# Performance work log

Hardware: AMD Instinct MI355X
Metric: run time of the kernel (lower is better)

Reference implementation:

```python
import jax, jax.numpy as jnp
import numpy as np

B, L, N, P = 64, 512, 321, 720   # batch, seq_len, enc_in, pred_len
E, R, CID, H = 8, 32, 32, 64     # experts, rank, channel_identity_dim, router hidden


def setup_inputs() -> dict:
    key = jax.random.key(0)
    ks = jax.random.split(key, 9)
    return {
        "x": jax.random.normal(ks[0], (B, L, N), dtype=jnp.float32),
        # per-channel identity embedding for the router
        "ident": jax.random.normal(ks[1], (N, CID), dtype=jnp.float32) * 0.02,
        # router MLP: CID -> H -> E
        "rw1": jax.random.normal(ks[2], (CID, H), dtype=jnp.float32) * (1.0 / np.sqrt(CID)),
        "rb1": jnp.zeros((H,), dtype=jnp.float32),
        "rw2": jax.random.normal(ks[3], (H, E), dtype=jnp.float32) * (1.0 / np.sqrt(H)),
        "rb2": jnp.zeros((E,), dtype=jnp.float32),
        # low-rank experts: L -> R -> P
        "w1": jax.random.normal(ks[4], (E, L, R), dtype=jnp.float32) * (1.0 / np.sqrt(L)),
        "w2": jax.random.normal(ks[5], (E, R, P), dtype=jnp.float32) * (1.0 / np.sqrt(R)),
        "b": jnp.zeros((E, P), dtype=jnp.float32),
    }


def reference(x, ident, rw1, rb1, rw2, rb2, w1, w2, b):
    # RevIN-style normalization over the time dim (torch std is unbiased, ddof=1)
    mean = jnp.mean(x, axis=1, keepdims=True)                    # [B,1,N]
    std = jnp.std(x, axis=1, keepdims=True, ddof=1) + 1e-6       # [B,1,N]
    xn = ((x - mean) / std).transpose(0, 2, 1)                   # [B,N,L]

    # per-channel MoE router (soft routing over experts)
    hidden = jax.nn.relu(ident @ rw1 + rb1)                      # [N,H]
    gate = jax.nn.softmax(hidden @ rw2 + rb2, axis=-1)           # [N,E]

    # low-rank expert projections L -> R -> P
    h = jnp.einsum('bnl,elr->bner', xn, w1)                      # [B,N,E,R]
    y = jnp.einsum('bner,erp->bnep', h, w2) + b                  # [B,N,E,P]
    y = jnp.einsum('bnep,ne->bnp', y, gate)                      # [B,N,P]

    pred = y.transpose(0, 2, 1)                                  # [B,P,N]
    return pred * std + mean
```

## Files before the change

kernel.cpp:

```cpp
#include <hip/hip_runtime.h>
#include <math.h>

#define B_ 64
#define L_ 512
#define N_ 321
#define P_ 720
#define E_ 8
#define R_ 32
#define CID_ 32
#define H_ 64
#define ER_ 256
#define KB2 288
#define HGROWS 384

typedef __attribute__((ext_vector_type(8))) short bf16x8;
typedef __attribute__((ext_vector_type(4))) float f32x4;
typedef __attribute__((ext_vector_type(8))) unsigned short u16x8;
typedef __attribute__((ext_vector_type(4))) unsigned short u16x4;

#define OFF_GATE 0
#define OFF_CS1  2568
#define OFF_W1K  2824
#define OFF_W2X  68360
#define OFF_HG   172040

__device__ __forceinline__ unsigned short f2bf(float f) {
    unsigned u = __float_as_uint(f);
    u += 0x7fffu + ((u >> 16) & 1u);
    return (unsigned short)(u >> 16);
}
__device__ __forceinline__ float bf2f(unsigned short h) {
    return __uint_as_float(((unsigned)h) << 16);
}

__global__ void router_kernel(const float* __restrict__ ident,
                              const float* __restrict__ rw1, const float* __restrict__ rb1,
                              const float* __restrict__ rw2, const float* __restrict__ rb2,
                              float* __restrict__ gate) {
    int n = blockIdx.x;
    int t = threadIdx.x;
    __shared__ float hid[H_];
    __shared__ float lg[E_];
    float acc = rb1[t];
    #pragma unroll
    for (int c = 0; c < CID_; ++c)
        acc = fmaf(ident[n*CID_ + c], rw1[c*H_ + t], acc);
    hid[t] = fmaxf(acc, 0.f);
    __syncthreads();
    if (t < E_) {
        float a = rb2[t];
        #pragma unroll
        for (int h = 0; h < H_; ++h) a = fmaf(hid[h], rw2[h*E_ + t], a);
        lg[t] = a;
    }
    __syncthreads();
    if (t == 0) {
        float m = lg[0];
        #pragma unroll
        for (int e = 1; e < E_; ++e) m = fmaxf(m, lg[e]);
        float s = 0.f, ex[E_];
        #pragma unroll
        for (int e = 0; e < E_; ++e) { ex[e] = expf(lg[e] - m); s += ex[e]; }
        float inv = 1.f / s;
        #pragma unroll
        for (int e = 0; e < E_; ++e) gate[n*E_ + e] = ex[e] * inv;
    }
}

__global__ void prep_kernel(const float* __restrict__ w1, const float* __restrict__ w2,
                            const float* __restrict__ bias,
                            unsigned short* __restrict__ w1k, unsigned short* __restrict__ w2x,
                            float* __restrict__ cs1) {
    __shared__ float red[16][32];
    int bid = blockIdx.x, t = threadIdx.x;
    if (bid < 128) {
        #pragma unroll
        for (int r = 0; r < 2; ++r) {
            int g = bid*1024 + r*512 + t;
            int er = g >> 9, l = g & 511;
            w1k[g] = f2bf(w1[(size_t)(er >> 5)*(L_*R_) + (size_t)l*R_ + (er & 31)]);
        }
    } else if (bid < 848) {
        int p = bid - 128;
        if (t < KB2) {
            unsigned short v;
            if (t < ER_)            v = f2bf(w2[(size_t)t*P_ + p]);
            else if (t < ER_ + E_)  v = f2bf(bias[(size_t)(t - ER_)*P_ + p]);
            else if (t == ER_ + E_) v = 0x3f80;
            else                    v = 0;
            w2x[(size_t)p*KB2 + t] = v;
        }
    } else {
        int e = bid - 848;
        int q = t >> 5, r = t & 31;
        float s = 0.f;
        for (int l = q; l < L_; l += 16)
            s += bf2f(f2bf(w1[(size_t)e*(L_*R_) + (size_t)l*R_ + r]));
        red[q][r] = s;
        __syncthreads();
        if (q == 0) {
            #pragma unroll
            for (int qq = 1; qq < 16; ++qq) s += red[qq][r];
            cs1[e*32 + r] = s;
        }
    }
}

__global__ __launch_bounds__(512, 4) void gemm1_kernel(
        const float* __restrict__ x, const unsigned short* __restrict__ w1k,
        const float* __restrict__ gate, const float* __restrict__ cs1,
        unsigned short* __restrict__ hg) {
    __shared__ unsigned short buf[2][64][128];
    __shared__ float red1[8][64], red2[8][64];
    __shared__ float meanS[64], sdS[64];

    const int bid = blockIdx.x;
    const int xcd = bid & 7;
    const int idx = bid >> 3;
    const int b   = (xcd << 3) + idx / 6;
    const int n0  = (idx % 6) * 64;

    const int tid  = threadIdx.x;
    const int lane = tid & 63;
    const int wave = tid >> 6;
    const int l15  = lane & 15;
    const int kgrp = lane >> 4;

    const int xn  = lane;
    const int gn  = n0 + xn;
    const int gnc = (gn < N_) ? gn : (N_ - 1);
    const float* xp = x + (size_t)b*L_*N_ + gnc;
    const int swz = (xn & 7) << 4;
    char* myrow0 = (char*)&buf[0][xn][0];
    char* myrow1 = (char*)&buf[1][xn][0];

    const unsigned short* apA = w1k + (size_t)(wave*32 + l15)*L_;
    const unsigned short* apB = w1k + (size_t)(wave*32 + 16 + l15)*L_;
    const int rsw = (l15 & 7) << 4;

    float s1 = 0.f, s2 = 0.f;
    float v[16];
    f32x4 acc[2][4];
    #pragma unroll
    for (int i = 0; i < 2; ++i)
        #pragma unroll
        for (int j = 0; j < 4; ++j) acc[i][j] = (f32x4){0.f,0.f,0.f,0.f};

#define LOADV(rd_) {                                                            \
    const int kb = (rd_)*128 + wave*16;                                         \
    _Pragma("unroll")                                                           \
    for (int i_ = 0; i_ < 16; ++i_)                                             \
        v[i_] = xp[(size_t)(kb + i_)*N_]; }
#define STOREV(rd_) {                                                           \
    char* dst = ((rd_) & 1) ? myrow1 : myrow0;                                  \
    u16x8 pk0, pk1;                                                             \
    _Pragma("unroll")                                                           \
    for (int i_ = 0; i_ < 8; ++i_) {                                            \
        s1 += v[i_]; s2 = fmaf(v[i_], v[i_], s2); pk0[i_] = f2bf(v[i_]); }      \
    _Pragma("unroll")                                                           \
    for (int i_ = 0; i_ < 8; ++i_) {                                            \
        float f_ = v[8+i_];                                                     \
        s1 += f_; s2 = fmaf(f_, f_, s2); pk1[i_] = f2bf(f_); }                  \
    *(u16x8*)(dst + ((wave*32)      ^ swz)) = pk0;                              \
    *(u16x8*)(dst + ((wave*32 + 16) ^ swz)) = pk1; }

    LOADV(0);
    STOREV(0);
    __syncthreads();

    bf16x8 af[4][2];
#define LDA(s_, kk_) { af[s_][0] = *(const bf16x8*)&apA[(kk_)*32 + kgrp*8];      \
                       af[s_][1] = *(const bf16x8*)&apB[(kk_)*32 + kgrp*8]; }
    LDA(0, 0); LDA(1, 1);

    #pragma unroll
    for (int rd = 0; rd < 4; ++rd) {
        if (rd < 3) LOADV(rd + 1);
        const unsigned short (*cb)[128] = buf[rd & 1];
        #pragma unroll
        for (int ks = 0; ks < 4; ++ks) {
            const int kk = rd*4 + ks;
            if (kk + 2 < 16) LDA((kk + 2) & 3, kk + 2);
            const int cbyte = ks*64 + kgrp*16;
            bf16x8 bfr[4];
            #pragma unroll
            for (int fn = 0; fn < 4; ++fn)
                bfr[fn] = *(const bf16x8*)((const char*)&cb[fn*16 + l15][0] + (cbyte ^ rsw));
            #pragma unroll
            for (int fn = 0; fn < 4; ++fn) {
                acc[0][fn] = __builtin_amdgcn_mfma_f32_16x16x32_bf16(af[kk & 3][0], bfr[fn], acc[0][fn], 0, 0, 0);
                acc[1][fn] = __builtin_amdgcn_mfma_f32_16x16x32_bf16(af[kk & 3][1], bfr[fn], acc[1][fn], 0, 0, 0);
            }
        }
        if (rd < 3) STOREV(rd + 1);
        __syncthreads();
    }
#undef LDA
#undef LOADV
#undef STOREV

    red1[wave][xn] = s1;
    red2[wave][xn] = s2;
    __syncthreads();
    if (tid < 64) {
        float a = 0.f, qq = 0.f;
        #pragma unroll
        for (int kk = 0; kk < 8; ++kk) { a += red1[kk][tid]; qq += red2[kk][tid]; }
        float mean = a * (1.f/L_);
        float var = (qq - (float)L_*mean*mean) * (1.f/(L_-1));
        var = fmaxf(var, 0.f);
        meanS[tid] = mean;
        sdS[tid]   = sqrtf(var) + 1e-6f;
    }
    __syncthreads();

    unsigned short* hgb = hg + ((size_t)b * HGROWS + n0) * KB2;
    #pragma unroll
    for (int fm = 0; fm < 2; ++fm) {
        int er0 = wave*32 + fm*16 + kgrp*4;
        int e = er0 >> 5;
        f32x4 c4 = *(const f32x4*)&cs1[er0];
        #pragma unroll
        for (int fn = 0; fn < 4; ++fn) {
            int nl = fn*16 + l15;
            int gnn = n0 + nl; if (gnn > N_-1) gnn = N_-1;
            float g = gate[gnn*E_ + e];
            float m = meanS[nl];
            u16x4 pk;
            #pragma unroll
            for (int j = 0; j < 4; ++j)
                pk[j] = f2bf(g * (acc[fm][fn][j] - m * c4[j]));
            *(u16x4*)&hgb[(size_t)nl*KB2 + er0] = pk;
        }
    }
    {
        int nl = tid >> 3, seg = tid & 7;
        int gnn = n0 + nl; if (gnn > N_-1) gnn = N_-1;
        float sd = sdS[nl], m = meanS[nl];
        u16x4 pk;
        #pragma unroll
        for (int jj = 0; jj < 4; ++jj) {
            int k = seg*4 + jj;
            float vv = (k < E_) ? gate[gnn*E_ + k] * sd : ((k == E_) ? m : 0.f);
            pk[jj] = f2bf(vv);
        }
        *(u16x4*)&hgb[(size_t)nl*KB2 + ER_ + seg*4] = pk;
    }
}

#define HGS 296
__global__ __launch_bounds__(512, 6) void gemm2_kernel(
        const unsigned short* __restrict__ hg, const unsigned short* __restrict__ w2x,
        float* __restrict__ out) {
    __shared__ __align__(16) char smem[64 * HGS * 2];
    unsigned short* hgL = (unsigned short*)smem;
    const int bid = blockIdx.x;
    const int xcd = bid & 7;
    const int idx = bid >> 3;
    const int b   = (xcd << 3) + idx / 36;
    const int rem = idx % 36;
    const int p0  = (rem / 6) * 128;
    const int n0  = (rem % 6) * 64;

    const int tid  = threadIdx.x;
    const int lane = tid & 63;
    const int wave = tid >> 6;
    const int l15  = lane & 15;
    const int kgrp = lane >> 4;

    const unsigned short* hgb = hg + ((size_t)b * HGROWS + n0) * KB2;
    #pragma unroll
    for (int it = 0; it < 5; ++it) {
        int c = tid + it*512;
        if (c < 64*36) {
            int row = c / 36, col = c % 36;
            *(u16x8*)&hgL[(size_t)row*HGS + col*8] =
                *(const u16x8*)&hgb[(size_t)row*KB2 + col*8];
        }
    }
    __syncthreads();

    int prow = p0 + wave*16 + l15; if (prow > P_-1) prow = P_-1;
    const unsigned short* ap = w2x + (size_t)prow*KB2;
    f32x4 o[4];
    #pragma unroll
    for (int j = 0; j < 4; ++j) o[j] = (f32x4){0.f,0.f,0.f,0.f};
    #pragma unroll
    for (int ks = 0; ks < 9; ++ks) {
        bf16x8 afr = *(const bf16x8*)&ap[ks*32 + kgrp*8];
        #pragma unroll
        for (int fn = 0; fn < 4; ++fn) {
            bf16x8 bfr = *(const bf16x8*)&hgL[(size_t)(fn*16 + l15)*HGS + ks*32 + kgrp*8];
            o[fn] = __builtin_amdgcn_mfma_f32_16x16x32_bf16(afr, bfr, o[fn], 0, 0, 0);
        }
    }
    __syncthreads();

    float* patch = (float*)smem + wave * 1088;
    #pragma unroll
    for (int fn = 0; fn < 4; ++fn)
        #pragma unroll
        for (int j = 0; j < 4; ++j)
            patch[(kgrp*4 + j)*68 + fn*16 + l15] = o[fn][j];
    const int pw0 = p0 + wave*16;
    #pragma unroll
    for (int pass = 0; pass < 4; ++pass) {
        int ploc = pass*4 + kgrp;
        f32x4 v = *(const f32x4*)&patch[ploc*68 + l15*4];
        int p = pw0 + ploc;
        int n = n0 + l15*4;
        if (p < P_) {
            float* orow = out + ((size_t)b*P_ + p)*N_;
            if (n + 3 < N_) {
                *(f32x4*)&orow[n] = v;
            } else {
                #pragma unroll
                for (int j = 0; j < 4; ++j)
                    if (n + j < N_) orow[n + j] = v[j];
            }
        }
    }
}

extern "C" void kernel_launch(void* const* d_in, const int* in_sizes, int n_in,
                              void* d_out, int out_size, void* d_ws, size_t ws_size,
                              hipStream_t stream) {
    const float* x     = (const float*)d_in[0];
    const float* ident = (const float*)d_in[1];
    const float* rw1   = (const float*)d_in[2];
    const float* rb1   = (const float*)d_in[3];
    const float* rw2   = (const float*)d_in[4];
    const float* rb2   = (const float*)d_in[5];
    const float* w1    = (const float*)d_in[6];
    const float* w2    = (const float*)d_in[7];
    const float* bias  = (const float*)d_in[8];
    float* out = (float*)d_out;
    float* ws  = (float*)d_ws;

    float* gate = ws + OFF_GATE;
    float* cs1  = ws + OFF_CS1;
    unsigned short* w1k = (unsigned short*)(ws + OFF_W1K);
    unsigned short* w2x = (unsigned short*)(ws + OFF_W2X);
    unsigned short* hg  = (unsigned short*)(ws + OFF_HG);

    router_kernel<<<N_, 64, 0, stream>>>(ident, rw1, rb1, rw2, rb2, gate);
    prep_kernel<<<856, 512, 0, stream>>>(w1, w2, bias, w1k, w2x, cs1);
    gemm1_kernel<<<dim3(384), 512, 0, stream>>>(x, w1k, gate, cs1, hg);
    gemm2_kernel<<<dim3(2304), 512, 0, stream>>>(hg, w2x, out);
}
```

Before: 66.61 us.

## Fuse router into prep kernel and split gemm1 across expert halves

The router computation moves into extra blocks of the prep kernel, which removes one kernel launch. gemm1 now splits the 256 expert-rank outputs into two halves of 128 across separate blocks, giving 768 blocks instead of 384. The accumulators per thread are halved and launch bounds allow 6 blocks per CU, which is meant to raise occupancy and parallelism. The cost is that each block now reloads and re-reduces the x tile, so reads of x and the mean/std work are duplicated.

```diff
diff --git a/kernel.cpp b/kernel.cpp
--- a/kernel.cpp
+++ b/kernel.cpp
@@ -33,45 +33,16 @@
     return __uint_as_float(((unsigned)h) << 16);
 }
 
-__global__ void router_kernel(const float* __restrict__ ident,
-                              const float* __restrict__ rw1, const float* __restrict__ rb1,
-                              const float* __restrict__ rw2, const float* __restrict__ rb2,
-                              float* __restrict__ gate) {
-    int n = blockIdx.x;
-    int t = threadIdx.x;
+__global__ void prep_kernel(const float* __restrict__ w1, const float* __restrict__ w2,
+                            const float* __restrict__ bias,
+                            const float* __restrict__ ident,
+                            const float* __restrict__ rw1, const float* __restrict__ rb1,
+                            const float* __restrict__ rw2, const float* __restrict__ rb2,
+                            unsigned short* __restrict__ w1k, unsigned short* __restrict__ w2x,
+                            float* __restrict__ cs1, float* __restrict__ gate) {
+    __shared__ float red[16][32];
     __shared__ float hid[H_];
     __shared__ float lg[E_];
-    float acc = rb1[t];
-    #pragma unroll
-    for (int c = 0; c < CID_; ++c)
-        acc = fmaf(ident[n*CID_ + c], rw1[c*H_ + t], acc);
-    hid[t] = fmaxf(acc, 0.f);
-    __syncthreads();
-    if (t < E_) {
-        float a = rb2[t];
-        #pragma unroll
-        for (int h = 0; h < H_; ++h) a = fmaf(hid[h], rw2[h*E_ + t], a);
-        lg[t] = a;
-    }
-    __syncthreads();
-    if (t == 0) {
-        float m = lg[0];
-        #pragma unroll
-        for (int e = 1; e < E_; ++e) m = fmaxf(m, lg[e]);
-        float s = 0.f, ex[E_];
-        #pragma unroll
-        for (int e = 0; e < E_; ++e) { ex[e] = expf(lg[e] - m); s += ex[e]; }
-        float inv = 1.f / s;
-        #pragma unroll
-        for (int e = 0; e < E_; ++e) gate[n*E_ + e] = ex[e] * inv;
-    }
-}
-
-__global__ void prep_kernel(const float* __restrict__ w1, const float* __restrict__ w2,
-                            const float* __restrict__ bias,
-                            unsigned short* __restrict__ w1k, unsigned short* __restrict__ w2x,
-                            float* __restrict__ cs1) {
-    __shared__ float red[16][32];
     int bid = blockIdx.x, t = threadIdx.x;
     if (bid < 128) {
         #pragma unroll
@@ -90,7 +61,7 @@
             else                    v = 0;
             w2x[(size_t)p*KB2 + t] = v;
         }
-    } else {
+    } else if (bid < 856) {
         int e = bid - 848;
         int q = t >> 5, r = t & 31;
         float s = 0.f;
@@ -103,10 +74,38 @@
             for (int qq = 1; qq < 16; ++qq) s += red[qq][r];
             cs1[e*32 + r] = s;
         }
-    }
-}
-
-__global__ __launch_bounds__(512, 4) void gemm1_kernel(
+    } else {
+        int n = bid - 856;
+        if (t < H_) {
+            float acc = rb1[t];
+            #pragma unroll
+            for (int c = 0; c < CID_; ++c)
+                acc = fmaf(ident[n*CID_ + c], rw1[c*H_ + t], acc);
+            hid[t] = fmaxf(acc, 0.f);
+        }
+        __syncthreads();
+        if (t < E_) {
+            float a = rb2[t];
+            #pragma unroll
+            for (int h = 0; h < H_; ++h) a = fmaf(hid[h], rw2[h*E_ + t], a);
+            lg[t] = a;
+        }
+        __syncthreads();
+        if (t == 0) {
+            float m = lg[0];
+            #pragma unroll
+            for (int e = 1; e < E_; ++e) m = fmaxf(m, lg[e]);
+            float s = 0.f, ex[E_];
+            #pragma unroll
+            for (int e = 0; e < E_; ++e) { ex[e] = expf(lg[e] - m); s += ex[e]; }
+            float inv = 1.f / s;
+            #pragma unroll
+            for (int e = 0; e < E_; ++e) gate[n*E_ + e] = ex[e] * inv;
+        }
+    }
+}
+
+__global__ __launch_bounds__(512, 6) void gemm1_kernel(
         const float* __restrict__ x, const unsigned short* __restrict__ w1k,
         const float* __restrict__ gate, const float* __restrict__ cs1,
         unsigned short* __restrict__ hg) {
@@ -117,8 +116,12 @@
     const int bid = blockIdx.x;
     const int xcd = bid & 7;
     const int idx = bid >> 3;
-    const int b   = (xcd << 3) + idx / 6;
-    const int n0  = (idx % 6) * 64;
+    const int b   = (xcd << 3) + idx / 12;
+    const int rem = idx % 12;
+    const int nt  = rem >> 1;
+    const int eq  = rem & 1;
+    const int n0  = nt * 64;
+    const int m0  = eq * 128;
 
     const int tid  = threadIdx.x;
     const int lane = tid & 63;
@@ -134,17 +137,14 @@
     char* myrow0 = (char*)&buf[0][xn][0];
     char* myrow1 = (char*)&buf[1][xn][0];
 
-    const unsigned short* apA = w1k + (size_t)(wave*32 + l15)*L_;
-    const unsigned short* apB = w1k + (size_t)(wave*32 + 16 + l15)*L_;
+    const unsigned short* apA = w1k + (size_t)(m0 + wave*16 + l15)*L_;
     const int rsw = (l15 & 7) << 4;
 
     float s1 = 0.f, s2 = 0.f;
     float v[16];
-    f32x4 acc[2][4];
-    #pragma unroll
-    for (int i = 0; i < 2; ++i)
-        #pragma unroll
-        for (int j = 0; j < 4; ++j) acc[i][j] = (f32x4){0.f,0.f,0.f,0.f};
+    f32x4 acc[4];
+    #pragma unroll
+    for (int j = 0; j < 4; ++j) acc[j] = (f32x4){0.f,0.f,0.f,0.f};
 
 #define LOADV(rd_) {                                                            \
     const int kb = (rd_)*128 + wave*16;                                         \
@@ -168,9 +168,8 @@
     STOREV(0);
     __syncthreads();
 
-    bf16x8 af[4][2];
-#define LDA(s_, kk_) { af[s_][0] = *(const bf16x8*)&apA[(kk_)*32 + kgrp*8];      \
-                       af[s_][1] = *(const bf16x8*)&apB[(kk_)*32 + kgrp*8]; }
+    bf16x8 af[4];
+#define LDA(s_, kk_) af[s_] = *(const bf16x8*)&apA[(kk_)*32 + kgrp*8];
     LDA(0, 0); LDA(1, 1);
 
     #pragma unroll
@@ -187,10 +186,8 @@
             for (int fn = 0; fn < 4; ++fn)
                 bfr[fn] = *(const bf16x8*)((const char*)&cb[fn*16 + l15][0] + (cbyte ^ rsw));
             #pragma unroll
-            for (int fn = 0; fn < 4; ++fn) {
-                acc[0][fn] = __builtin_amdgcn_mfma_f32_16x16x32_bf16(af[kk & 3][0], bfr[fn], acc[0][fn], 0, 0, 0);
-                acc[1][fn] = __builtin_amdgcn_mfma_f32_16x16x32_bf16(af[kk & 3][1], bfr[fn], acc[1][fn], 0, 0, 0);
-            }
+            for (int fn = 0; fn < 4; ++fn)
+                acc[fn] = __builtin_amdgcn_mfma_f32_16x16x32_bf16(af[kk & 3], bfr[fn], acc[fn], 0, 0, 0);
         }
         if (rd < 3) STOREV(rd + 1);
         __syncthreads();
@@ -215,9 +212,8 @@
     __syncthreads();
 
     unsigned short* hgb = hg + ((size_t)b * HGROWS + n0) * KB2;
-    #pragma unroll
-    for (int fm = 0; fm < 2; ++fm) {
-        int er0 = wave*32 + fm*16 + kgrp*4;
+    {
+        int er0 = m0 + wave*16 + kgrp*4;
         int e = er0 >> 5;
         f32x4 c4 = *(const f32x4*)&cs1[er0];
         #pragma unroll
@@ -229,11 +225,11 @@
             u16x4 pk;
             #pragma unroll
             for (int j = 0; j < 4; ++j)
-                pk[j] = f2bf(g * (acc[fm][fn][j] - m * c4[j]));
+                pk[j] = f2bf(g * (acc[fn][j] - m * c4[j]));
             *(u16x4*)&hgb[(size_t)nl*KB2 + er0] = pk;
         }
     }
-    {
+    if (eq == 1) {
         int nl = tid >> 3, seg = tid & 7;
         int gnn = n0 + nl; if (gnn > N_-1) gnn = N_-1;
         float sd = sdS[nl], m = meanS[nl];
@@ -343,8 +339,8 @@
     unsigned short* w2x = (unsigned short*)(ws + OFF_W2X);
     unsigned short* hg  = (unsigned short*)(ws + OFF_HG);
 
-    router_kernel<<<N_, 64, 0, stream>>>(ident, rw1, rb1, rw2, rb2, gate);
-    prep_kernel<<<856, 512, 0, stream>>>(w1, w2, bias, w1k, w2x, cs1);
-    gemm1_kernel<<<dim3(384), 512, 0, stream>>>(x, w1k, gate, cs1, hg);
+    prep_kernel<<<856 + N_, 512, 0, stream>>>(w1, w2, bias, ident, rw1, rb1,
+                                              rw2, rb2, w1k, w2x, cs1, gate);
+    gemm1_kernel<<<dim3(768), 512, 0, stream>>>(x, w1k, gate, cs1, hg);
     gemm2_kernel<<<dim3(2304), 512, 0, stream>>>(hg, w2x, out);
 }
```

New measurement: 60.97 us. 8.5% less time.

## Pre-transpose x to bf16 in a separate kernel and merge router into prep

Applied to the files above, without the earlier changes.

Adds a kernel that transposes x from [B,L,N] into a bf16 [B,384,L] buffer through padded shared memory, so gemm1 can read contiguous rows instead of strided columns. gemm1 then loads each 32-channel tile in one pass, computes the mean/std with shuffles and runs a single unpipelined MFMA loop over 704 blocks. The router kernel is folded into the prep kernel as extra blocks, removing one launch. The change adds an extra bf16 copy of x written to and read back from global memory. Statistics are now computed from bf16-rounded values rather than fp32.

```diff
diff --git a/kernel.cpp b/kernel.cpp
--- a/kernel.cpp
+++ b/kernel.cpp
@@ -12,17 +12,20 @@
 #define ER_ 256
 #define KB2 288
 #define HGROWS 384
+#define TRS 338
 
 typedef __attribute__((ext_vector_type(8))) short bf16x8;
 typedef __attribute__((ext_vector_type(4))) float f32x4;
 typedef __attribute__((ext_vector_type(8))) unsigned short u16x8;
 typedef __attribute__((ext_vector_type(4))) unsigned short u16x4;
+typedef __attribute__((ext_vector_type(2))) unsigned short u16x2;
 
 #define OFF_GATE 0
 #define OFF_CS1  2568
 #define OFF_W1K  2824
 #define OFF_W2X  68360
-#define OFF_HG   172040
+#define OFF_XT   172040
+#define OFF_HG   6463496
 
 __device__ __forceinline__ unsigned short f2bf(float f) {
     unsigned u = __float_as_uint(f);
@@ -33,45 +36,16 @@
     return __uint_as_float(((unsigned)h) << 16);
 }
 
-__global__ void router_kernel(const float* __restrict__ ident,
-                              const float* __restrict__ rw1, const float* __restrict__ rb1,
-                              const float* __restrict__ rw2, const float* __restrict__ rb2,
-                              float* __restrict__ gate) {
-    int n = blockIdx.x;
-    int t = threadIdx.x;
+__global__ void prep_kernel(const float* __restrict__ w1, const float* __restrict__ w2,
+                            const float* __restrict__ bias,
+                            const float* __restrict__ ident,
+                            const float* __restrict__ rw1, const float* __restrict__ rb1,
+                            const float* __restrict__ rw2, const float* __restrict__ rb2,
+                            unsigned short* __restrict__ w1k, unsigned short* __restrict__ w2x,
+                            float* __restrict__ cs1, float* __restrict__ gate) {
+    __shared__ float red[16][32];
     __shared__ float hid[H_];
     __shared__ float lg[E_];
-    float acc = rb1[t];
-    #pragma unroll
-    for (int c = 0; c < CID_; ++c)
-        acc = fmaf(ident[n*CID_ + c], rw1[c*H_ + t], acc);
-    hid[t] = fmaxf(acc, 0.f);
-    __syncthreads();
-    if (t < E_) {
-        float a = rb2[t];
-        #pragma unroll
-        for (int h = 0; h < H_; ++h) a = fmaf(hid[h], rw2[h*E_ + t], a);
-        lg[t] = a;
-    }
-    __syncthreads();
-    if (t == 0) {
-        float m = lg[0];
-        #pragma unroll
-        for (int e = 1; e < E_; ++e) m = fmaxf(m, lg[e]);
-        float s = 0.f, ex[E_];
-        #pragma unroll
-        for (int e = 0; e < E_; ++e) { ex[e] = expf(lg[e] - m); s += ex[e]; }
-        float inv = 1.f / s;
-        #pragma unroll
-        for (int e = 0; e < E_; ++e) gate[n*E_ + e] = ex[e] * inv;
-    }
-}
-
-__global__ void prep_kernel(const float* __restrict__ w1, const float* __restrict__ w2,
-                            const float* __restrict__ bias,
-                            unsigned short* __restrict__ w1k, unsigned short* __restrict__ w2x,
-                            float* __restrict__ cs1) {
-    __shared__ float red[16][32];
     int bid = blockIdx.x, t = threadIdx.x;
     if (bid < 128) {
         #pragma unroll
@@ -90,7 +64,7 @@
             else                    v = 0;
             w2x[(size_t)p*KB2 + t] = v;
         }
-    } else {
+    } else if (bid < 856) {
         int e = bid - 848;
         int q = t >> 5, r = t & 31;
         float s = 0.f;
@@ -103,22 +77,92 @@
             for (int qq = 1; qq < 16; ++qq) s += red[qq][r];
             cs1[e*32 + r] = s;
         }
+    } else {
+        int n = bid - 856;
+        if (t < H_) {
+            float acc = rb1[t];
+            #pragma unroll
+            for (int c = 0; c < CID_; ++c)
+                acc = fmaf(ident[n*CID_ + c], rw1[c*H_ + t], acc);
+            hid[t] = fmaxf(acc, 0.f);
+        }
+        __syncthreads();
+        if (t < E_) {
+            float a = rb2[t];
+            #pragma unroll
+            for (int h = 0; h < H_; ++h) a = fmaf(hid[h], rw2[h*E_ + t], a);
+            lg[t] = a;
+        }
+        __syncthreads();
+        if (t == 0) {
+            float m = lg[0];
+            #pragma unroll
+            for (int e = 1; e < E_; ++e) m = fmaxf(m, lg[e]);
+            float s = 0.f, ex[E_];
+            #pragma unroll
+            for (int e = 0; e < E_; ++e) { ex[e] = expf(lg[e] - m); s += ex[e]; }
+            float inv = 1.f / s;
+            #pragma unroll
+            for (int e = 0; e < E_; ++e) gate[n*E_ + e] = ex[e] * inv;
+        }
+    }
+}
+
+__global__ __launch_bounds__(512) void prepx2_kernel(
+        const float* __restrict__ x, unsigned short* __restrict__ xT) {
+    __shared__ unsigned short tr[64 * TRS];
+    const int bid = blockIdx.x;
+    const int b   = bid >> 3;
+    const int kc  = bid & 7;
+    const int tid = threadIdx.x;
+    const int lane = tid & 63;
+    const int wave = tid >> 6;
+
+    const float* xb = x + (size_t)b*L_*N_ + (size_t)kc*64*N_;
+    #pragma unroll
+    for (int rr = 0; rr < 8; ++rr) {
+        const int r = wave*8 + rr;
+        const float* row = xb + (size_t)r*N_;
+        #pragma unroll
+        for (int it = 0; it < 6; ++it) {
+            int c = it*64 + lane;
+            if (c < N_)        tr[r*TRS + c] = f2bf(row[c]);
+            else if (c < 336)  tr[r*TRS + c] = 0;
+        }
+    }
+    __syncthreads();
+
+    #pragma unroll
+    for (int pass = 0; pass < 6; ++pass) {
+        int n = pass*64 + (tid >> 3);
+        int chunk = tid & 7;
+        if (n < 336) {
+            u16x8 pk;
+            #pragma unroll
+            for (int j = 0; j < 8; ++j) pk[j] = tr[(chunk*8 + j)*TRS + n];
+            *(u16x8*)&xT[((size_t)b*HGROWS + n)*L_ + kc*64 + chunk*8] = pk;
+        }
+    }
+    if (tid < 384) {
+        int n = 336 + (tid >> 3);
+        int chunk = tid & 7;
+        u16x8 z = {0,0,0,0,0,0,0,0};
+        *(u16x8*)&xT[((size_t)b*HGROWS + n)*L_ + kc*64 + chunk*8] = z;
     }
 }
 
 __global__ __launch_bounds__(512, 4) void gemm1_kernel(
-        const float* __restrict__ x, const unsigned short* __restrict__ w1k,
+        const unsigned short* __restrict__ xT, const unsigned short* __restrict__ w1k,
         const float* __restrict__ gate, const float* __restrict__ cs1,
         unsigned short* __restrict__ hg) {
-    __shared__ unsigned short buf[2][64][128];
-    __shared__ float red1[8][64], red2[8][64];
-    __shared__ float meanS[64], sdS[64];
+    __shared__ __align__(16) unsigned short xL[32 * 512];
+    __shared__ float meanS[32], sdS[32];
 
     const int bid = blockIdx.x;
     const int xcd = bid & 7;
     const int idx = bid >> 3;
-    const int b   = (xcd << 3) + idx / 6;
-    const int n0  = (idx % 6) * 64;
+    const int b   = (xcd << 3) + idx / 11;
+    const int n0  = (idx % 11) * 32;
 
     const int tid  = threadIdx.x;
     const int lane = tid & 63;
@@ -126,93 +170,67 @@
     const int l15  = lane & 15;
     const int kgrp = lane >> 4;
 
-    const int xn  = lane;
-    const int gn  = n0 + xn;
-    const int gnc = (gn < N_) ? gn : (N_ - 1);
-    const float* xp = x + (size_t)b*L_*N_ + gnc;
-    const int swz = (xn & 7) << 4;
-    char* myrow0 = (char*)&buf[0][xn][0];
-    char* myrow1 = (char*)&buf[1][xn][0];
+    const int n_loc = tid >> 4;
+    const int seg   = tid & 15;
+    const unsigned short* xrow = xT + ((size_t)b*HGROWS + n0 + n_loc)*L_ + seg*32;
+    float s1 = 0.f, s2 = 0.f;
+    {
+        u16x8 st[4];
+        #pragma unroll
+        for (int j = 0; j < 4; ++j) {
+            st[j] = *(const u16x8*)&xrow[j*8];
+            #pragma unroll
+            for (int q = 0; q < 8; ++q) {
+                float f = bf2f(st[j][q]);
+                s1 += f; s2 = fmaf(f, f, s2);
+            }
+        }
+        const int swzw = (n_loc & 7) << 4;
+        char* dst = (char*)xL + n_loc*1024;
+        #pragma unroll
+        for (int j = 0; j < 4; ++j)
+            *(u16x8*)(dst + ((seg*64 + j*16) ^ swzw)) = st[j];
+    }
+    __syncthreads();
+    #pragma unroll
+    for (int m = 1; m <= 8; m <<= 1) {
+        s1 += __shfl_xor(s1, m);
+        s2 += __shfl_xor(s2, m);
+    }
+    if (seg == 0) {
+        float mean = s1 * (1.f/L_);
+        float var = (s2 - (float)L_*mean*mean) * (1.f/(L_-1));
+        meanS[n_loc] = mean;
+        sdS[n_loc]   = sqrtf(fmaxf(var, 0.f)) + 1e-6f;
+    }
+    __syncthreads();
 
     const unsigned short* apA = w1k + (size_t)(wave*32 + l15)*L_;
     const unsigned short* apB = w1k + (size_t)(wave*32 + 16 + l15)*L_;
     const int rsw = (l15 & 7) << 4;
 
-    float s1 = 0.f, s2 = 0.f;
-    float v[16];
-    f32x4 acc[2][4];
+    f32x4 acc[2][2];
     #pragma unroll
     for (int i = 0; i < 2; ++i)
         #pragma unroll
-        for (int j = 0; j < 4; ++j) acc[i][j] = (f32x4){0.f,0.f,0.f,0.f};
-
-#define LOADV(rd_) {                                                            \
-    const int kb = (rd_)*128 + wave*16;                                         \
-    _Pragma("unroll")                                                           \
-    for (int i_ = 0; i_ < 16; ++i_)                                             \
-        v[i_] = xp[(size_t)(kb + i_)*N_]; }
-#define STOREV(rd_) {                                                           \
-    char* dst = ((rd_) & 1) ? myrow1 : myrow0;                                  \
-    u16x8 pk0, pk1;                                                             \
-    _Pragma("unroll")                                                           \
-    for (int i_ = 0; i_ < 8; ++i_) {                                            \
-        s1 += v[i_]; s2 = fmaf(v[i_], v[i_], s2); pk0[i_] = f2bf(v[i_]); }      \
-    _Pragma("unroll")                                                           \
-    for (int i_ = 0; i_ < 8; ++i_) {                                            \
-        float f_ = v[8+i_];                                                     \
-        s1 += f_; s2 = fmaf(f_, f_, s2); pk1[i_] = f2bf(f_); }                  \
-    *(u16x8*)(dst + ((wave*32)      ^ swz)) = pk0;                              \
-    *(u16x8*)(dst + ((wave*32 + 16) ^ swz)) = pk1; }
-
-    LOADV(0);
-    STOREV(0);
-    __syncthreads();
+        for (int j = 0; j < 2; ++j) acc[i][j] = (f32x4){0.f,0.f,0.f,0.f};
 
     bf16x8 af[4][2];
 #define LDA(s_, kk_) { af[s_][0] = *(const bf16x8*)&apA[(kk_)*32 + kgrp*8];      \
                        af[s_][1] = *(const bf16x8*)&apB[(kk_)*32 + kgrp*8]; }
     LDA(0, 0); LDA(1, 1);
-
-    #pragma unroll
-    for (int rd = 0; rd < 4; ++rd) {
-        if (rd < 3) LOADV(rd + 1);
-        const unsigned short (*cb)[128] = buf[rd & 1];
-        #pragma unroll
-        for (int ks = 0; ks < 4; ++ks) {
-            const int kk = rd*4 + ks;
-            if (kk + 2 < 16) LDA((kk + 2) & 3, kk + 2);
-            const int cbyte = ks*64 + kgrp*16;
-            bf16x8 bfr[4];
-            #pragma unroll
-            for (int fn = 0; fn < 4; ++fn)
-                bfr[fn] = *(const bf16x8*)((const char*)&cb[fn*16 + l15][0] + (cbyte ^ rsw));
-            #pragma unroll
-            for (int fn = 0; fn < 4; ++fn) {
-                acc[0][fn] = __builtin_amdgcn_mfma_f32_16x16x32_bf16(af[kk & 3][0], bfr[fn], acc[0][fn], 0, 0, 0);
-                acc[1][fn] = __builtin_amdgcn_mfma_f32_16x16x32_bf16(af[kk & 3][1], bfr[fn], acc[1][fn], 0, 0, 0);
-            }
-        }
-        if (rd < 3) STOREV(rd + 1);
-        __syncthreads();
+    #pragma unroll
+    for (int ks = 0; ks < 16; ++ks) {
+        if (ks + 2 < 16) LDA((ks + 2) & 3, ks + 2);
+        const int cb = (ks*64 + kgrp*16);
+        bf16x8 b0 = *(const bf16x8*)((char*)xL + l15*1024        + (cb ^ rsw));
+        bf16x8 b1 = *(const bf16x8*)((char*)xL + (16 + l15)*1024 + (cb ^ rsw));
+        acc[0][0] = __builtin_amdgcn_mfma_f32_16x16x32_bf16(af[ks & 3][0], b0, acc[0][0], 0, 0, 0);
+        acc[0][1] = __builtin_amdgcn_mfma_f32_16x16x32_bf16(af[ks & 3][0], b1, acc[0][1], 0, 0, 0);
+        acc[1][0] = __builtin_amdgcn_mfma_f32_16x16x32_bf16(af[ks & 3][1], b0, acc[1][0], 0, 0, 0);
+        acc[1][1] = __builtin_amdgcn_mfma_f32_16x16x32_bf16(af[ks & 3][1], b1, acc[1][1], 0, 0, 0);
     }
 #undef LDA
-#undef LOADV
-#undef STOREV
-
-    red1[wave][xn] = s1;
-    red2[wave][xn] = s2;
-    __syncthreads();
-    if (tid < 64) {
-        float a = 0.f, qq = 0.f;
-        #pragma unroll
-        for (int kk = 0; kk < 8; ++kk) { a += red1[kk][tid]; qq += red2[kk][tid]; }
-        float mean = a * (1.f/L_);
-        float var = (qq - (float)L_*mean*mean) * (1.f/(L_-1));
-        var = fmaxf(var, 0.f);
-        meanS[tid] = mean;
-        sdS[tid]   = sqrtf(var) + 1e-6f;
-    }
-    __syncthreads();
 
     unsigned short* hgb = hg + ((size_t)b * HGROWS + n0) * KB2;
     #pragma unroll
@@ -221,7 +239,7 @@
         int e = er0 >> 5;
         f32x4 c4 = *(const f32x4*)&cs1[er0];
         #pragma unroll
-        for (int fn = 0; fn < 4; ++fn) {
+        for (int fn = 0; fn < 2; ++fn) {
             int nl = fn*16 + l15;
             int gnn = n0 + nl; if (gnn > N_-1) gnn = N_-1;
             float g = gate[gnn*E_ + e];
@@ -234,17 +252,17 @@
         }
     }
     {
-        int nl = tid >> 3, seg = tid & 7;
+        int nl = tid >> 4, sg = tid & 15;
         int gnn = n0 + nl; if (gnn > N_-1) gnn = N_-1;
         float sd = sdS[nl], m = meanS[nl];
-        u16x4 pk;
-        #pragma unroll
-        for (int jj = 0; jj < 4; ++jj) {
-            int k = seg*4 + jj;
+        u16x2 pk;
+        #pragma unroll
+        for (int jj = 0; jj < 2; ++jj) {
+            int k = sg*2 + jj;
             float vv = (k < E_) ? gate[gnn*E_ + k] * sd : ((k == E_) ? m : 0.f);
             pk[jj] = f2bf(vv);
         }
-        *(u16x4*)&hgb[(size_t)nl*KB2 + ER_ + seg*4] = pk;
+        *(u16x2*)&hgb[(size_t)nl*KB2 + ER_ + sg*2] = pk;
     }
 }
 
@@ -341,10 +359,12 @@
     float* cs1  = ws + OFF_CS1;
     unsigned short* w1k = (unsigned short*)(ws + OFF_W1K);
     unsigned short* w2x = (unsigned short*)(ws + OFF_W2X);
+    unsigned short* xT  = (unsigned short*)(ws + OFF_XT);
     unsigned short* hg  = (unsigned short*)(ws + OFF_HG);
 
-    router_kernel<<<N_, 64, 0, stream>>>(ident, rw1, rb1, rw2, rb2, gate);
-    prep_kernel<<<856, 512, 0, stream>>>(w1, w2, bias, w1k, w2x, cs1);
-    gemm1_kernel<<<dim3(384), 512, 0, stream>>>(x, w1k, gate, cs1, hg);
+    prep_kernel<<<856 + N_, 512, 0, stream>>>(w1, w2, bias, ident, rw1, rb1,
+                                              rw2, rb2, w1k, w2x, cs1, gate);
+    prepx2_kernel<<<512, 512, 0, stream>>>(x, xT);
+    gemm1_kernel<<<dim3(704), 512, 0, stream>>>(xT, w1k, gate, cs1, hg);
     gemm2_kernel<<<dim3(2304), 512, 0, stream>>>(hg, w2x, out);
 }
```

Result: slower. 79.88 us (+19.9%).

## Stream x tiles into LDS via global_load_lds and fold router into prep

Applied to the files above, without the earlier changes.

Replaces the register-staged strided loads of x in gemm1 with direct global-to-LDS DMA loads (global_load_lds) into a double-buffered fp32 tile. A separate conversion pass then computes the statistics and packs bf16 into a swizzled tile, with the K loop split into 8 rounds of 64. It also merges the router kernel into the prep kernel as extra blocks, saving one launch. The change is meant to hide load latency and cut register pressure. In exchange it adds more barriers per round and relies on hand-placed vmcnt waits.

```diff
diff --git a/kernel.cpp b/kernel.cpp
--- a/kernel.cpp
+++ b/kernel.cpp
@@ -33,45 +33,21 @@
     return __uint_as_float(((unsigned)h) << 16);
 }
 
-__global__ void router_kernel(const float* __restrict__ ident,
-                              const float* __restrict__ rw1, const float* __restrict__ rb1,
-                              const float* __restrict__ rw2, const float* __restrict__ rb2,
-                              float* __restrict__ gate) {
-    int n = blockIdx.x;
-    int t = threadIdx.x;
+#define GLD4(gsrc, ldst)                                                        \
+    __builtin_amdgcn_global_load_lds(                                           \
+        (const __attribute__((address_space(1))) unsigned*)(gsrc),              \
+        (__attribute__((address_space(3))) unsigned*)(ldst), 4, 0, 0)
+
+__global__ void prep_kernel(const float* __restrict__ w1, const float* __restrict__ w2,
+                            const float* __restrict__ bias,
+                            const float* __restrict__ ident,
+                            const float* __restrict__ rw1, const float* __restrict__ rb1,
+                            const float* __restrict__ rw2, const float* __restrict__ rb2,
+                            unsigned short* __restrict__ w1k, unsigned short* __restrict__ w2x,
+                            float* __restrict__ cs1, float* __restrict__ gate) {
+    __shared__ float red[16][32];
     __shared__ float hid[H_];
     __shared__ float lg[E_];
-    float acc = rb1[t];
-    #pragma unroll
-    for (int c = 0; c < CID_; ++c)
-        acc = fmaf(ident[n*CID_ + c], rw1[c*H_ + t], acc);
-    hid[t] = fmaxf(acc, 0.f);
-    __syncthreads();
-    if (t < E_) {
-        float a = rb2[t];
-        #pragma unroll
-        for (int h = 0; h < H_; ++h) a = fmaf(hid[h], rw2[h*E_ + t], a);
-        lg[t] = a;
-    }
-    __syncthreads();
-    if (t == 0) {
-        float m = lg[0];
-        #pragma unroll
-        for (int e = 1; e < E_; ++e) m = fmaxf(m, lg[e]);
-        float s = 0.f, ex[E_];
-        #pragma unroll
-        for (int e = 0; e < E_; ++e) { ex[e] = expf(lg[e] - m); s += ex[e]; }
-        float inv = 1.f / s;
-        #pragma unroll
-        for (int e = 0; e < E_; ++e) gate[n*E_ + e] = ex[e] * inv;
-    }
-}
-
-__global__ void prep_kernel(const float* __restrict__ w1, const float* __restrict__ w2,
-                            const float* __restrict__ bias,
-                            unsigned short* __restrict__ w1k, unsigned short* __restrict__ w2x,
-                            float* __restrict__ cs1) {
-    __shared__ float red[16][32];
     int bid = blockIdx.x, t = threadIdx.x;
     if (bid < 128) {
         #pragma unroll
@@ -90,7 +66,7 @@
             else                    v = 0;
             w2x[(size_t)p*KB2 + t] = v;
         }
-    } else {
+    } else if (bid < 856) {
         int e = bid - 848;
         int q = t >> 5, r = t & 31;
         float s = 0.f;
@@ -103,6 +79,34 @@
             for (int qq = 1; qq < 16; ++qq) s += red[qq][r];
             cs1[e*32 + r] = s;
         }
+    } else {
+        int n = bid - 856;
+        if (t < H_) {
+            float acc = rb1[t];
+            #pragma unroll
+            for (int c = 0; c < CID_; ++c)
+                acc = fmaf(ident[n*CID_ + c], rw1[c*H_ + t], acc);
+            hid[t] = fmaxf(acc, 0.f);
+        }
+        __syncthreads();
+        if (t < E_) {
+            float a = rb2[t];
+            #pragma unroll
+            for (int h = 0; h < H_; ++h) a = fmaf(hid[h], rw2[h*E_ + t], a);
+            lg[t] = a;
+        }
+        __syncthreads();
+        if (t == 0) {
+            float m = lg[0];
+            #pragma unroll
+            for (int e = 1; e < E_; ++e) m = fmaxf(m, lg[e]);
+            float s = 0.f, ex[E_];
+            #pragma unroll
+            for (int e = 0; e < E_; ++e) { ex[e] = expf(lg[e] - m); s += ex[e]; }
+            float inv = 1.f / s;
+            #pragma unroll
+            for (int e = 0; e < E_; ++e) gate[n*E_ + e] = ex[e] * inv;
+        }
     }
 }
 
@@ -110,7 +114,8 @@
         const float* __restrict__ x, const unsigned short* __restrict__ w1k,
         const float* __restrict__ gate, const float* __restrict__ cs1,
         unsigned short* __restrict__ hg) {
-    __shared__ unsigned short buf[2][64][128];
+    __shared__ __align__(16) float fs[2][64][64];
+    __shared__ __align__(16) unsigned short bf[64][64];
     __shared__ float red1[8][64], red2[8][64];
     __shared__ float meanS[64], sdS[64];
 
@@ -126,46 +131,42 @@
     const int l15  = lane & 15;
     const int kgrp = lane >> 4;
 
-    const int xn  = lane;
-    const int gn  = n0 + xn;
+    const int gn  = n0 + lane;
     const int gnc = (gn < N_) ? gn : (N_ - 1);
-    const float* xp = x + (size_t)b*L_*N_ + gnc;
-    const int swz = (xn & 7) << 4;
-    char* myrow0 = (char*)&buf[0][xn][0];
-    char* myrow1 = (char*)&buf[1][xn][0];
+    const float* xb = x + (size_t)b*L_*N_ + gnc;
+
+#define DMA(rd_) {                                                              \
+    const int kb = (rd_)*64 + wave*8;                                           \
+    _Pragma("unroll")                                                           \
+    for (int i_ = 0; i_ < 8; ++i_)                                              \
+        GLD4(xb + (size_t)(kb + i_)*N_, &fs[(rd_) & 1][wave*8 + i_][0]); }
+
+#define CONV(rd_) {                                                             \
+    const int cur = (rd_) & 1;                                                  \
+    float vv[8];                                                                \
+    _Pragma("unroll")                                                           \
+    for (int i_ = 0; i_ < 8; ++i_) vv[i_] = fs[cur][wave*8 + i_][lane];         \
+    u16x8 pk;                                                                   \
+    _Pragma("unroll")                                                           \
+    for (int i_ = 0; i_ < 8; ++i_) {                                            \
+        s1 += vv[i_]; s2 = fmaf(vv[i_], vv[i_], s2); pk[i_] = f2bf(vv[i_]); }   \
+    *(u16x8*)((char*)&bf[lane][0] + ((wave*16) ^ ((lane & 7) << 4))) = pk; }
+
+    float s1 = 0.f, s2 = 0.f;
+    f32x4 acc[2][4];
+    #pragma unroll
+    for (int i = 0; i < 2; ++i)
+        #pragma unroll
+        for (int j = 0; j < 4; ++j) acc[i][j] = (f32x4){0.f,0.f,0.f,0.f};
 
     const unsigned short* apA = w1k + (size_t)(wave*32 + l15)*L_;
     const unsigned short* apB = w1k + (size_t)(wave*32 + 16 + l15)*L_;
     const int rsw = (l15 & 7) << 4;
 
-    float s1 = 0.f, s2 = 0.f;
-    float v[16];
-    f32x4 acc[2][4];
-    #pragma unroll
-    for (int i = 0; i < 2; ++i)
-        #pragma unroll
-        for (int j = 0; j < 4; ++j) acc[i][j] = (f32x4){0.f,0.f,0.f,0.f};
-
-#define LOADV(rd_) {                                                            \
-    const int kb = (rd_)*128 + wave*16;                                         \
-    _Pragma("unroll")                                                           \
-    for (int i_ = 0; i_ < 16; ++i_)                                             \
-        v[i_] = xp[(size_t)(kb + i_)*N_]; }
-#define STOREV(rd_) {                                                           \
-    char* dst = ((rd_) & 1) ? myrow1 : myrow0;                                  \
-    u16x8 pk0, pk1;                                                             \
-    _Pragma("unroll")                                                           \
-    for (int i_ = 0; i_ < 8; ++i_) {                                            \
-        s1 += v[i_]; s2 = fmaf(v[i_], v[i_], s2); pk0[i_] = f2bf(v[i_]); }      \
-    _Pragma("unroll")                                                           \
-    for (int i_ = 0; i_ < 8; ++i_) {                                            \
-        float f_ = v[8+i_];                                                     \
-        s1 += f_; s2 = fmaf(f_, f_, s2); pk1[i_] = f2bf(f_); }                  \
-    *(u16x8*)(dst + ((wave*32)      ^ swz)) = pk0;                              \
-    *(u16x8*)(dst + ((wave*32 + 16) ^ swz)) = pk1; }
-
-    LOADV(0);
-    STOREV(0);
+    DMA(0); DMA(1);
+    asm volatile("s_waitcnt vmcnt(8)" ::: "memory");
+    __syncthreads();
+    CONV(0);
     __syncthreads();
 
     bf16x8 af[4][2];
@@ -174,33 +175,40 @@
     LDA(0, 0); LDA(1, 1);
 
     #pragma unroll
-    for (int rd = 0; rd < 4; ++rd) {
-        if (rd < 3) LOADV(rd + 1);
-        const unsigned short (*cb)[128] = buf[rd & 1];
-        #pragma unroll
-        for (int ks = 0; ks < 4; ++ks) {
-            const int kk = rd*4 + ks;
+    for (int rd = 0; rd < 8; ++rd) {
+        #pragma unroll
+        for (int ks = 0; ks < 2; ++ks) {
+            const int kk = rd*2 + ks;
             if (kk + 2 < 16) LDA((kk + 2) & 3, kk + 2);
             const int cbyte = ks*64 + kgrp*16;
             bf16x8 bfr[4];
             #pragma unroll
             for (int fn = 0; fn < 4; ++fn)
-                bfr[fn] = *(const bf16x8*)((const char*)&cb[fn*16 + l15][0] + (cbyte ^ rsw));
+                bfr[fn] = *(const bf16x8*)((const char*)&bf[fn*16 + l15][0] + (cbyte ^ rsw));
             #pragma unroll
             for (int fn = 0; fn < 4; ++fn) {
                 acc[0][fn] = __builtin_amdgcn_mfma_f32_16x16x32_bf16(af[kk & 3][0], bfr[fn], acc[0][fn], 0, 0, 0);
                 acc[1][fn] = __builtin_amdgcn_mfma_f32_16x16x32_bf16(af[kk & 3][1], bfr[fn], acc[1][fn], 0, 0, 0);
             }
         }
-        if (rd < 3) STOREV(rd + 1);
-        __syncthreads();
+        if (rd < 7) {
+            if (rd + 2 < 8) {
+                DMA(rd + 2);
+                asm volatile("s_waitcnt vmcnt(8)" ::: "memory");
+            } else {
+                asm volatile("s_waitcnt vmcnt(0)" ::: "memory");
+            }
+            __syncthreads();
+            CONV(rd + 1);
+            __syncthreads();
+        }
     }
 #undef LDA
-#undef LOADV
-#undef STOREV
-
-    red1[wave][xn] = s1;
-    red2[wave][xn] = s2;
+#undef DMA
+#undef CONV
+
+    red1[wave][lane] = s1;
+    red2[wave][lane] = s2;
     __syncthreads();
     if (tid < 64) {
         float a = 0.f, qq = 0.f;
@@ -343,8 +351,8 @@
     unsigned short* w2x = (unsigned short*)(ws + OFF_W2X);
     unsigned short* hg  = (unsigned short*)(ws + OFF_HG);
 
-    router_kernel<<<N_, 64, 0, stream>>>(ident, rw1, rb1, rw2, rb2, gate);
-    prep_kernel<<<856, 512, 0, stream>>>(w1, w2, bias, w1k, w2x, cs1);
+    prep_kernel<<<856 + N_, 512, 0, stream>>>(w1, w2, bias, ident, rw1, rb1,
+                                              rw2, rb2, w1k, w2x, cs1, gate);
     gemm1_kernel<<<dim3(384), 512, 0, stream>>>(x, w1k, gate, cs1, hg);
     gemm2_kernel<<<dim3(2304), 512, 0, stream>>>(hg, w2x, out);
 }
```

Measured after the change: 64.34 us. 3.4% less time.
